# Kernel optimization log

Hardware: AMD Instinct MI355X
Metric: run time of the kernel (lower is better)

Reference implementation:

```python
import jax, jax.numpy as jnp
import numpy as np

N, E, DIN, H, CHID, COUT, S = 20000, 320000, 128, 4, 64, 64, 32
EPS_BN = 1e-5


def setup_inputs() -> dict:
    key = jax.random.key(0)
    ks = jax.random.split(key, 20)
    g = lambda k, shp, s=0.1: jax.random.normal(k, shp, dtype=jnp.float32) * s
    return {
        "x": jax.random.normal(ks[0], (N, DIN), dtype=jnp.float32),
        "edge_index": jax.random.randint(ks[1], (2, E), 0, N, dtype=jnp.int32),
        "struct_feat": jax.random.normal(ks[2], (N, S), dtype=jnp.float32),
        # GATConv (layer 1)
        "W1": g(ks[3], (H * CHID, DIN)),
        "att_src1": g(ks[4], (1, H, CHID)),
        "att_dst1": g(ks[5], (1, H, CHID)),
        "bias1": jnp.zeros((CHID,), jnp.float32),
        # HybridGateGATLayer (layer 2)
        "W2": g(ks[6], (H * COUT, CHID)),
        "att_src2": g(ks[7], (1, H, COUT)),
        "att_dst2": g(ks[8], (1, H, COUT)),
        "bias2": jnp.zeros((COUT,), jnp.float32),
        "Wt": g(ks[9], (1, S)),
        "bt": jnp.zeros((1,), jnp.float32),
        "We1": g(ks[10], (8, 4), 0.5),
        "be1": jnp.zeros((8,), jnp.float32),
        "We2": g(ks[11], (1, 8), 0.5),
        "be2": jnp.zeros((1,), jnp.float32),
        "betas": jnp.array([1.15, 0.85, 0.1, 0.08, 0.12], jnp.float32),
    }


def _seg_softmax(logits, seg, n):
    m = jax.ops.segment_max(logits, seg, num_segments=n)
    m = jnp.where(jnp.isfinite(m), m, 0.0)
    ex = jnp.exp(logits - m[seg])
    s = jax.ops.segment_sum(ex, seg, num_segments=n)
    return ex / (s[seg] + 1e-16)


def _cos(a, b):
    na = jnp.maximum(jnp.linalg.norm(a, axis=-1), 1e-8)
    nb = jnp.maximum(jnp.linalg.norm(b, axis=-1), 1e-8)
    return (a * b).sum(-1) / (na * nb)


def reference(x, edge_index, struct_feat, W1, att_src1, att_dst1, bias1,
              W2, att_src2, att_dst2, bias2, Wt, bt, We1, be1, We2, be2, betas):
    n = x.shape[0]
    src0, dst0 = edge_index[0], edge_index[1]
    # ---- layer 1: standard GATConv with self loops, concat=False (head mean) ----
    loop = jnp.arange(n, dtype=src0.dtype)
    src = jnp.concatenate([src0, loop])
    dst = jnp.concatenate([dst0, loop])
    h = (x @ W1.T).reshape(n, H, CHID)
    a_s = (h * att_src1).sum(-1)  # [N,H]
    a_d = (h * att_dst1).sum(-1)
    al = jax.nn.leaky_relu(a_s[src] + a_d[dst], 0.2)  # [E+N,H]
    alpha1 = _seg_softmax(al, dst, n)
    out1 = jax.ops.segment_sum(h[src] * alpha1[..., None], dst, num_segments=n)
    h1 = jax.nn.relu(out1.mean(1) + bias1)  # [N,CHID]
    # batch norm (affine=False, batch stats, biased var)
    mu = h1.mean(0)
    var = ((h1 - mu) ** 2).mean(0)
    h1 = (h1 - mu) / jnp.sqrt(var + EPS_BN)
    # ---- layer 2: HybridGateGATLayer (no self loops) ----
    x2 = (h1 @ W2.T).reshape(n, H, COUT)
    node_trust = jax.nn.sigmoid(struct_feat @ Wt.T + bt).squeeze(-1)  # [N]
    as2 = (x2 * att_src2).sum(-1)
    ad2 = (x2 * att_dst2).sum(-1)
    j, i = src0, dst0
    alpha_raw = jax.nn.leaky_relu(as2[j] + ad2[i], 0.2)  # [E,H]
    struct_sim = _cos(struct_feat[j], struct_feat[i])  # [E]
    xf = x2.reshape(n, H * COUT)
    feat_sim = _cos(xf[j], xf[i])
    agreement = struct_sim * feat_sim
    conflict = jnp.abs(struct_sim - feat_sim)
    cues = jnp.stack([struct_sim, feat_sim, agreement, conflict], axis=-1)  # [E,4]
    gate = (jax.nn.relu(cues @ We1.T + be1) @ We2.T + be2).squeeze(-1)
    edge_bonus = jax.nn.sigmoid(gate) * jax.nn.relu(agreement)
    edge_trust = jnp.sqrt(jnp.clip(node_trust[j] * node_trust[i], 0.0))
    trust_bonus = edge_trust * jax.nn.relu(0.5 * (struct_sim + feat_sim))
    gate_logit = (betas[0] * struct_sim + betas[1] * feat_sim + betas[2] * agreement
                  + betas[3] * edge_bonus + betas[4] * trust_bonus)
    alpha2 = _seg_softmax(alpha_raw + gate_logit[:, None], i, n)  # [E,H]
    out2 = jax.ops.segment_sum(x2[j] * alpha2[..., None], i, num_segments=n)
    return out2.mean(1) + bias2  # [N,COUT]
```

## Files before the change

### kernel.cpp

```cpp
#include <hip/hip_runtime.h>
#include <hip/hip_bf16.h>
#include <hip/hip_fp16.h>

#define C_DIN 128
#define C_H 4
#define C_CH 64
#define C_HC 256
#define C_S 32
#define MBLK 64

typedef __attribute__((ext_vector_type(8))) _Float16 half8;
typedef __attribute__((ext_vector_type(4))) float f32x4;

__device__ __forceinline__ float lrelu(float x) { return x >= 0.f ? x : 0.2f * x; }

__global__ void k_count(const int* __restrict__ dst, int* __restrict__ deg, int E) {
    int e = blockIdx.x * blockDim.x + threadIdx.x;
    if (e < E) atomicAdd(&deg[dst[e]], 1);
}

__global__ void k_scan(const int* __restrict__ deg, int* __restrict__ row_ptr,
                       int* __restrict__ cursor, int n) {
    __shared__ int part[1024];
    int t = threadIdx.x;
    const int C = (n + 1023) / 1024;
    int base = t * C;
    int s = 0;
    for (int k = 0; k < C; ++k) {
        int idx = base + k;
        if (idx < n) s += deg[idx];
    }
    part[t] = s;
    __syncthreads();
    for (int off = 1; off < 1024; off <<= 1) {
        int v = (t >= off) ? part[t - off] : 0;
        __syncthreads();
        part[t] += v;
        __syncthreads();
    }
    int run = (t == 0) ? 0 : part[t - 1];
    for (int k = 0; k < C; ++k) {
        int idx = base + k;
        if (idx < n) { row_ptr[idx] = run; cursor[idx] = run; run += deg[idx]; }
    }
    if (t == 1023) row_ptr[n] = run;
}

__global__ void k_scatter(const int* __restrict__ src, const int* __restrict__ dst,
                          int* __restrict__ cursor, int* __restrict__ adj_src, int E) {
    int e = blockIdx.x * blockDim.x + threadIdx.x;
    if (e < E) {
        int d = dst[e];
        int p = atomicAdd(&cursor[d], 1);
        adj_src[p] = src[e];
    }
}

__global__ void k_prepw(const float* __restrict__ W1, const float* __restrict__ W2,
                        _Float16* __restrict__ W1f, _Float16* __restrict__ W2f) {
    int i = blockIdx.x * blockDim.x + threadIdx.x;
    if (i < 4096) {
        int ks = i >> 10, rem = i & 1023, nt = rem >> 6, lpos = rem & 63;
        int c = nt * 16 + (lpos & 15);
        int kb = (ks * 4 + (lpos >> 4)) * 8;
        const float4* src = (const float4*)(W1 + (size_t)c * C_DIN + kb);
        float4 f0 = src[0], f1 = src[1];
        _Float16* dst = &W1f[(size_t)i * 8];
        dst[0] = (_Float16)f0.x; dst[1] = (_Float16)f0.y;
        dst[2] = (_Float16)f0.z; dst[3] = (_Float16)f0.w;
        dst[4] = (_Float16)f1.x; dst[5] = (_Float16)f1.y;
        dst[6] = (_Float16)f1.z; dst[7] = (_Float16)f1.w;
    } else if (i < 4096 + 2048) {
        int ii = i - 4096;
        int ks = ii >> 10, rem = ii & 1023, nt = rem >> 6, lpos = rem & 63;
        int c = nt * 16 + (lpos & 15);
        int kb = (ks * 4 + (lpos >> 4)) * 8;
        const float4* src = (const float4*)(W2 + (size_t)c * C_CH + kb);
        float4 f0 = src[0], f1 = src[1];
        _Float16* dst = &W2f[(size_t)ii * 8];
        dst[0] = (_Float16)f0.x; dst[1] = (_Float16)f0.y;
        dst[2] = (_Float16)f0.z; dst[3] = (_Float16)f0.w;
        dst[4] = (_Float16)f1.x; dst[5] = (_Float16)f1.y;
        dst[6] = (_Float16)f1.z; dst[7] = (_Float16)f1.w;
    }
}

__global__ __launch_bounds__(256) void k_gemm1(
    const float* __restrict__ x, const _Float16* __restrict__ W1f,
    const float* __restrict__ att_s, const float* __restrict__ att_d,
    __half* __restrict__ hh_out, float* __restrict__ a_s, float* __restrict__ a_d, int n) {
    __shared__ __align__(16) _Float16 as_[4 * 4 * 64 * 8];
    int t = threadIdx.x;
    int r0 = blockIdx.x * MBLK;
    {
        int row = t >> 2, q = t & 3;
        int rr = r0 + row;
        int mt = row >> 4, rl = row & 15;
        const float4* xrow = (const float4*)(x + (size_t)rr * C_DIN);
#pragma unroll
        for (int cc = 0; cc < 4; ++cc) {
            int ch = q * 4 + cc;
            float4 f0 = make_float4(0, 0, 0, 0), f1 = make_float4(0, 0, 0, 0);
            if (rr < n) { f0 = xrow[ch * 2]; f1 = xrow[ch * 2 + 1]; }
            int ks = ch >> 2, lg = ch & 3;
            _Float16* dst = &as_[(((ks * 4 + mt) * 64) + (lg * 16 + rl)) * 8];
            dst[0] = (_Float16)f0.x; dst[1] = (_Float16)f0.y;
            dst[2] = (_Float16)f0.z; dst[3] = (_Float16)f0.w;
            dst[4] = (_Float16)f1.x; dst[5] = (_Float16)f1.y;
            dst[6] = (_Float16)f1.z; dst[7] = (_Float16)f1.w;
        }
    }
    __syncthreads();
    int w = t >> 6, l = t & 63;
    const half8* Wv = (const half8*)W1f;
    f32x4 acc[4][4];
#pragma unroll
    for (int mt = 0; mt < 4; ++mt)
#pragma unroll
        for (int nt = 0; nt < 4; ++nt) acc[mt][nt] = (f32x4){0.f, 0.f, 0.f, 0.f};
#pragma unroll
    for (int ks = 0; ks < 4; ++ks) {
        half8 af[4], bf[4];
#pragma unroll
        for (int mt = 0; mt < 4; ++mt)
            af[mt] = *(const half8*)&as_[(((ks * 4 + mt) * 64) + l) * 8];
#pragma unroll
        for (int nt = 0; nt < 4; ++nt)
            bf[nt] = Wv[((ks * 16 + (w * 4 + nt)) * 64) + l];
#pragma unroll
        for (int mt = 0; mt < 4; ++mt)
#pragma unroll
            for (int nt = 0; nt < 4; ++nt)
                acc[mt][nt] = __builtin_amdgcn_mfma_f32_16x16x32_f16(af[mt], bf[nt],
                                                                     acc[mt][nt], 0, 0, 0);
    }
    int cl = l & 15, rg = l >> 4;
    float atv_s[4], atv_d[4];
#pragma unroll
    for (int nt = 0; nt < 4; ++nt) {
        atv_s[nt] = att_s[w * 64 + nt * 16 + cl];
        atv_d[nt] = att_d[w * 64 + nt * 16 + cl];
    }
#pragma unroll
    for (int mt = 0; mt < 4; ++mt) {
#pragma unroll
        for (int r = 0; r < 4; ++r) {
            int rr = r0 + mt * 16 + rg * 4 + r;
            float vs = 0.f, vd = 0.f;
#pragma unroll
            for (int nt = 0; nt < 4; ++nt) {
                float v = acc[mt][nt][r];
                vs += atv_s[nt] * v;
                vd += atv_d[nt] * v;
                if (rr < n)
                    hh_out[(size_t)rr * C_HC + w * 64 + nt * 16 + cl] = __float2half(v);
            }
#pragma unroll
            for (int off = 1; off < 16; off <<= 1) {
                vs += __shfl_xor(vs, off);
                vd += __shfl_xor(vd, off);
            }
            if (cl == 0 && rr < n) { a_s[rr * C_H + w] = vs; a_d[rr * C_H + w] = vd; }
        }
    }
}

__global__ __launch_bounds__(256) void k_layer1(
    const int* __restrict__ row_ptr, const int* __restrict__ adj_src,
    const __half* __restrict__ hhlf, const float* __restrict__ a_s,
    const float* __restrict__ a_d, const float* __restrict__ bias1,
    float* __restrict__ h1, int n) {
    int wid = (blockIdx.x * blockDim.x + threadIdx.x) >> 6;
    if (wid >= n) return;
    int l = threadIdx.x & 63, g = l >> 4, q = l & 15, h = q >> 2;
    int d = wid;
    int beg = row_ptr[d], end = row_ptr[d + 1];
    float adh = a_d[d * C_H + h];
    const float4* drow = (const float4*)(hhlf + (size_t)d * C_HC + q * 16);
    float4 d0 = drow[0], d1 = drow[1];
    float acc[16];
#pragma unroll
    for (int i = 0; i < 16; ++i) acc[i] = 0.f;
    float s = 0.f;
    if (g == 0) {
        float ps = expf(lrelu(a_s[d * C_H + h] + adh));
        const __half2* pa = (const __half2*)&d0;
        const __half2* pb = (const __half2*)&d1;
#pragma unroll
        for (int k = 0; k < 4; ++k) {
            float2 a = __half22float2(pa[k]);
            acc[k * 2] += ps * a.x; acc[k * 2 + 1] += ps * a.y;
            float2 b = __half22float2(pb[k]);
            acc[8 + k * 2] += ps * b.x; acc[8 + k * 2 + 1] += ps * b.y;
        }
        s += ps;
    }
    for (int cb = beg; cb < end; cb += 4) {
        int e = cb + g;
        bool act = e < end;
        int j = act ? adj_src[e] : d;
        const float4* jrow = (const float4*)(hhlf + (size_t)j * C_HC + q * 16);
        float4 r0 = jrow[0], r1 = jrow[1];
        float p = act ? expf(lrelu(a_s[j * C_H + h] + adh)) : 0.f;
        const __half2* pa = (const __half2*)&r0;
        const __half2* pb = (const __half2*)&r1;
#pragma unroll
        for (int k = 0; k < 4; ++k) {
            float2 a = __half22float2(pa[k]);
            acc[k * 2] += p * a.x; acc[k * 2 + 1] += p * a.y;
            float2 b = __half22float2(pb[k]);
            acc[8 + k * 2] += p * b.x; acc[8 + k * 2 + 1] += p * b.y;
        }
        s += p;
    }
#pragma unroll
    for (int off = 16; off <= 32; off <<= 1) {
#pragma unroll
        for (int i = 0; i < 16; ++i) acc[i] += __shfl_xor(acc[i], off);
        s += __shfl_xor(s, off);
    }
    float inv = 1.f / (s + 1e-16f);
#pragma unroll
    for (int i = 0; i < 16; ++i) acc[i] *= inv;
#pragma unroll
    for (int off = 4; off <= 8; off <<= 1) {
#pragma unroll
        for (int i = 0; i < 16; ++i) acc[i] += __shfl_xor(acc[i], off);
    }
    if (l < 4) {
#pragma unroll
        for (int i = 0; i < 16; ++i)
            h1[(size_t)d * C_CH + l * 16 + i] =
                fmaxf(acc[i] * 0.25f + bias1[l * 16 + i], 0.f);
    }
}

__global__ void k_bnstats(const float* __restrict__ h1, float* __restrict__ bn, int n) {
    int t = threadIdx.x;
    int c = t & 63, rg = t >> 6;
    float s = 0.f, s2 = 0.f;
    for (int r = blockIdx.x * 4 + rg; r < n; r += gridDim.x * 4) {
        float v = h1[(size_t)r * C_CH + c];
        s += v;
        s2 += v * v;
    }
    __shared__ float ls[256], ls2[256];
    ls[t] = s; ls2[t] = s2;
    __syncthreads();
    if (t < 64) {
        s = ls[t] + ls[t + 64] + ls[t + 128] + ls[t + 192];
        s2 = ls2[t] + ls2[t + 64] + ls2[t + 128] + ls2[t + 192];
        atomicAdd(&bn[c], s);
        atomicAdd(&bn[64 + c], s2);
    }
}

__global__ __launch_bounds__(256) void k_gemm2(
    const float* __restrict__ h1, const _Float16* __restrict__ W2f,
    const float* __restrict__ att_s, const float* __restrict__ att_d,
    const float* __restrict__ bn, __half* __restrict__ x2h,
    float* __restrict__ as2, float* __restrict__ ad2, float* __restrict__ nf, int n) {
    __shared__ __align__(16) _Float16 as_[2 * 4 * 64 * 8];
    __shared__ float nq[64][4];
    int t = threadIdx.x;
    int r0 = blockIdx.x * MBLK;
    {
        int row = t >> 2, q = t & 3;
        int rr = r0 + row;
        int mt = row >> 4, rl = row & 15;
        const float invN = 1.f / (float)n;
        const float4* hrow = (const float4*)(h1 + (size_t)rr * C_CH);
#pragma unroll
        for (int cc = 0; cc < 2; ++cc) {
            int ch = q * 2 + cc;
            float4 f0 = make_float4(0, 0, 0, 0), f1 = make_float4(0, 0, 0, 0);
            if (rr < n) { f0 = hrow[ch * 2]; f1 = hrow[ch * 2 + 1]; }
            float4 s0 = *(const float4*)&bn[ch * 8];
            float4 s1 = *(const float4*)&bn[ch * 8 + 4];
            float4 q0 = *(const float4*)&bn[64 + ch * 8];
            float4 q1 = *(const float4*)&bn[64 + ch * 8 + 4];
            float4 mu0 = make_float4(s0.x * invN, s0.y * invN, s0.z * invN, s0.w * invN);
            float4 mu1 = make_float4(s1.x * invN, s1.y * invN, s1.z * invN, s1.w * invN);
            float4 rs0 = make_float4(rsqrtf(q0.x * invN - mu0.x * mu0.x + 1e-5f),
                                     rsqrtf(q0.y * invN - mu0.y * mu0.y + 1e-5f),
                                     rsqrtf(q0.z * invN - mu0.z * mu0.z + 1e-5f),
                                     rsqrtf(q0.w * invN - mu0.w * mu0.w + 1e-5f));
            float4 rs1 = make_float4(rsqrtf(q1.x * invN - mu1.x * mu1.x + 1e-5f),
                                     rsqrtf(q1.y * invN - mu1.y * mu1.y + 1e-5f),
                                     rsqrtf(q1.z * invN - mu1.z * mu1.z + 1e-5f),
                                     rsqrtf(q1.w * invN - mu1.w * mu1.w + 1e-5f));
            int ks = ch >> 1, lg = ch & 1;
            ks = ch >> 2; lg = ch & 3;
            _Float16* dst = &as_[(((ks * 4 + mt) * 64) + (lg * 16 + rl)) * 8];
            dst[0] = (_Float16)((f0.x - mu0.x) * rs0.x);
            dst[1] = (_Float16)((f0.y - mu0.y) * rs0.y);
            dst[2] = (_Float16)((f0.z - mu0.z) * rs0.z);
            dst[3] = (_Float16)((f0.w - mu0.w) * rs0.w);
            dst[4] = (_Float16)((f1.x - mu1.x) * rs1.x);
            dst[5] = (_Float16)((f1.y - mu1.y) * rs1.y);
            dst[6] = (_Float16)((f1.z - mu1.z) * rs1.z);
            dst[7] = (_Float16)((f1.w - mu1.w) * rs1.w);
        }
    }
    __syncthreads();
    int w = t >> 6, l = t & 63;
    const half8* Wv = (const half8*)W2f;
    f32x4 acc[4][4];
#pragma unroll
    for (int mt = 0; mt < 4; ++mt)
#pragma unroll
        for (int nt = 0; nt < 4; ++nt) acc[mt][nt] = (f32x4){0.f, 0.f, 0.f, 0.f};
#pragma unroll
    for (int ks = 0; ks < 2; ++ks) {
        half8 af[4], bf[4];
#pragma unroll
        for (int mt = 0; mt < 4; ++mt)
            af[mt] = *(const half8*)&as_[(((ks * 4 + mt) * 64) + l) * 8];
#pragma unroll
        for (int nt = 0; nt < 4; ++nt)
            bf[nt] = Wv[((ks * 16 + (w * 4 + nt)) * 64) + l];
#pragma unroll
        for (int mt = 0; mt < 4; ++mt)
#pragma unroll
            for (int nt = 0; nt < 4; ++nt)
                acc[mt][nt] = __builtin_amdgcn_mfma_f32_16x16x32_f16(af[mt], bf[nt],
                                                                     acc[mt][nt], 0, 0, 0);
    }
    int cl = l & 15, rg = l >> 4;
    float atv_s[4], atv_d[4];
#pragma unroll
    for (int nt = 0; nt < 4; ++nt) {
        atv_s[nt] = att_s[w * 64 + nt * 16 + cl];
        atv_d[nt] = att_d[w * 64 + nt * 16 + cl];
    }
#pragma unroll
    for (int mt = 0; mt < 4; ++mt) {
#pragma unroll
        for (int r = 0; r < 4; ++r) {
            int rr = r0 + mt * 16 + rg * 4 + r;
            float vs = 0.f, vd = 0.f, vq = 0.f;
#pragma unroll
            for (int nt = 0; nt < 4; ++nt) {
                float v = acc[mt][nt][r];
                vs += atv_s[nt] * v;
                vd += atv_d[nt] * v;
                vq += v * v;
                if (rr < n)
                    x2h[(size_t)rr * C_HC + w * 64 + nt * 16 + cl] = __float2half(v);
            }
#pragma unroll
            for (int off = 1; off < 16; off <<= 1) {
                vs += __shfl_xor(vs, off);
                vd += __shfl_xor(vd, off);
                vq += __shfl_xor(vq, off);
            }
            if (cl == 0 && rr < n) {
                as2[rr * C_H + w] = vs;
                ad2[rr * C_H + w] = vd;
                nq[mt * 16 + rg * 4 + r][w] = vq;
            }
        }
    }
    __syncthreads();
    if (t < MBLK) {
        int rr = r0 + t;
        if (rr < n) {
            float qq = nq[t][0] + nq[t][1] + nq[t][2] + nq[t][3];
            nf[rr] = fmaxf(sqrtf(qq), 1e-8f);
        }
    }
}

__global__ void k_trust(const float* __restrict__ sf, const float* __restrict__ Wt,
                        const float* __restrict__ bt, float* __restrict__ trust,
                        float* __restrict__ ns, int n) {
    int i = blockIdx.x * blockDim.x + threadIdx.x;
    if (i >= n) return;
    const float4* r4 = (const float4*)(sf + (size_t)i * C_S);
    const float4* w4 = (const float4*)Wt;
    float d = 0.f, q = 0.f;
#pragma unroll
    for (int k = 0; k < 8; ++k) {
        float4 a = r4[k], w = w4[k];
        d += a.x * w.x + a.y * w.y + a.z * w.z + a.w * w.w;
        q += a.x * a.x + a.y * a.y + a.z * a.z + a.w * a.w;
    }
    trust[i] = 1.f / (1.f + expf(-(d + bt[0])));
    ns[i] = fmaxf(sqrtf(q), 1e-8f);
}

__global__ __launch_bounds__(256) void k_fused2(
    const int* __restrict__ row_ptr, const int* __restrict__ adj_src,
    const float* __restrict__ sf, const __half* __restrict__ x2h,
    const float* __restrict__ ns, const float* __restrict__ nf,
    const float* __restrict__ trust, const float* __restrict__ as2,
    const float* __restrict__ ad2, const float* __restrict__ We1,
    const float* __restrict__ be1, const float* __restrict__ We2,
    const float* __restrict__ be2, const float* __restrict__ betas,
    const float* __restrict__ bias2, float* __restrict__ out, int n) {
    int wid = (blockIdx.x * blockDim.x + threadIdx.x) >> 6;
    if (wid >= n) return;
    int l = threadIdx.x & 63, g = l >> 4, q = l & 15, h = q >> 2;
    int d = wid;
    int beg = row_ptr[d], end = row_ptr[d + 1];
    const float4* drow = (const float4*)(x2h + (size_t)d * C_HC + q * 16);
    float4 d0 = drow[0], d1 = drow[1];
    float2 sfd = *(const float2*)(sf + (size_t)d * C_S + q * 2);
    float ad2h = ad2[d * C_H + h];
    float nsd = ns[d], nfd = nf[d], trd = trust[d];
    float b20 = be2[0];
    float bt0 = betas[0], bt1 = betas[1], bt2 = betas[2], bt3 = betas[3], bt4 = betas[4];
    float acc[16];
#pragma unroll
    for (int i = 0; i < 16; ++i) acc[i] = 0.f;
    float s = 0.f;
    for (int cb = beg; cb < end; cb += 4) {
        int e = cb + g;
        bool act = e < end;
        int j = act ? adj_src[e] : d;
        const float4* jrow = (const float4*)(x2h + (size_t)j * C_HC + q * 16);
        float4 r0 = jrow[0], r1 = jrow[1];
        float2 sfj = *(const float2*)(sf + (size_t)j * C_S + q * 2);
        float fd = 0.f;
        {
            const __half2* pa = (const __half2*)&r0;
            const __half2* pb = (const __half2*)&d0;
#pragma unroll
            for (int k = 0; k < 4; ++k) {
                float2 a = __half22float2(pa[k]), b = __half22float2(pb[k]);
                fd += a.x * b.x + a.y * b.y;
            }
            const __half2* pc = (const __half2*)&r1;
            const __half2* pd = (const __half2*)&d1;
#pragma unroll
            for (int k = 0; k < 4; ++k) {
                float2 a = __half22float2(pc[k]), b = __half22float2(pd[k]);
                fd += a.x * b.x + a.y * b.y;
            }
        }
        float sd = sfj.x * sfd.x + sfj.y * sfd.y;
#pragma unroll
        for (int off = 1; off < 16; off <<= 1) {
            fd += __shfl_xor(fd, off);
            sd += __shfl_xor(sd, off);
        }
        float p = 0.f;
        if (act) {
            float ss = sd / (nsd * ns[j]);
            float fs = fd / (nfd * nf[j]);
            float agr = ss * fs;
            float con = fabsf(ss - fs);
            float gate = b20;
#pragma unroll
            for (int o = 0; o < 8; ++o) {
                float hdn = We1[o * 4 + 0] * ss + We1[o * 4 + 1] * fs +
                            We1[o * 4 + 2] * agr + We1[o * 4 + 3] * con + be1[o];
                gate += We2[o] * fmaxf(hdn, 0.f);
            }
            float eb = (1.f / (1.f + expf(-gate))) * fmaxf(agr, 0.f);
            float et = sqrtf(fmaxf(trd * trust[j], 0.f));
            float tb = et * fmaxf(0.5f * (ss + fs), 0.f);
            float glog = bt0 * ss + bt1 * fs + bt2 * agr + bt3 * eb + bt4 * tb;
            p = expf(lrelu(as2[j * C_H + h] + ad2h) + glog);
        }
        {
            const __half2* pa = (const __half2*)&r0;
            const __half2* pb = (const __half2*)&r1;
#pragma unroll
            for (int k = 0; k < 4; ++k) {
                float2 a = __half22float2(pa[k]);
                acc[k * 2] += p * a.x; acc[k * 2 + 1] += p * a.y;
                float2 b = __half22float2(pb[k]);
                acc[8 + k * 2] += p * b.x; acc[8 + k * 2 + 1] += p * b.y;
            }
        }
        s += p;
    }
#pragma unroll
    for (int off = 16; off <= 32; off <<= 1) {
#pragma unroll
        for (int i = 0; i < 16; ++i) acc[i] += __shfl_xor(acc[i], off);
        s += __shfl_xor(s, off);
    }
    float inv = 1.f / (s + 1e-16f);
#pragma unroll
    for (int i = 0; i < 16; ++i) acc[i] *= inv;
#pragma unroll
    for (int off = 4; off <= 8; off <<= 1) {
#pragma unroll
        for (int i = 0; i < 16; ++i) acc[i] += __shfl_xor(acc[i], off);
    }
    if (l < 4) {
#pragma unroll
        for (int i = 0; i < 16; ++i)
            out[(size_t)d * C_CH + l * 16 + i] = acc[i] * 0.25f + bias2[l * 16 + i];
    }
}

static inline size_t al256(size_t x) { return (x + 255) & ~(size_t)255; }

extern "C" void kernel_launch(void* const* d_in, const int* in_sizes, int n_in,
                              void* d_out, int out_size, void* d_ws, size_t ws_size,
                              hipStream_t stream) {
    const float* x      = (const float*)d_in[0];
    const int*   ei     = (const int*)d_in[1];
    const float* sf     = (const float*)d_in[2];
    const float* W1     = (const float*)d_in[3];
    const float* atts1  = (const float*)d_in[4];
    const float* attd1  = (const float*)d_in[5];
    const float* bias1  = (const float*)d_in[6];
    const float* W2     = (const float*)d_in[7];
    const float* atts2  = (const float*)d_in[8];
    const float* attd2  = (const float*)d_in[9];
    const float* bias2  = (const float*)d_in[10];
    const float* Wt     = (const float*)d_in[11];
    const float* bt     = (const float*)d_in[12];
    const float* We1    = (const float*)d_in[13];
    const float* be1    = (const float*)d_in[14];
    const float* We2    = (const float*)d_in[15];
    const float* be2    = (const float*)d_in[16];
    const float* betas  = (const float*)d_in[17];

    const int N = in_sizes[0] / C_DIN;
    const int E = in_sizes[1] / 2;
    const int* srcs = ei;
    const int* dsts = ei + E;

    char* p = (char*)d_ws;
    size_t off = 0;
    auto take = [&](size_t bytes) { char* r = p + off; off = al256(off + bytes); return r; };
    __half* hhlf  = (__half*)take((size_t)N * C_HC * 2);
    float* h1     = (float*)take((size_t)N * C_CH * 4);
    float* a_s1   = (float*)take((size_t)N * C_H * 4);
    float* a_d1   = (float*)take((size_t)N * C_H * 4);
    float* nf     = (float*)take((size_t)N * 4);
    float* ns     = (float*)take((size_t)N * 4);
    float* trust  = (float*)take((size_t)N * 4);
    int*   deg    = (int*)take((size_t)N * 4);
    int*   rowp   = (int*)take((size_t)(N + 1) * 4);
    int*   cursor = (int*)take((size_t)N * 4);
    int*   adj_s  = (int*)take((size_t)E * 4);
    _Float16* W1f = (_Float16*)take(4096 * 8 * 2);
    _Float16* W2f = (_Float16*)take(2048 * 8 * 2);
    float* bn     = (float*)take(128 * 4);
    (void)ws_size;
    __half* x2h = hhlf;
    float* as2  = a_s1;
    float* ad2  = a_d1;

    hipMemsetAsync(deg, 0, (size_t)N * 4, stream);
    hipMemsetAsync(bn, 0, 128 * 4, stream);

    k_prepw<<<24, 256, 0, stream>>>(W1, W2, W1f, W2f);
    k_count<<<(E + 255) / 256, 256, 0, stream>>>(dsts, deg, E);
    k_scan<<<1, 1024, 0, stream>>>(deg, rowp, cursor, N);
    k_scatter<<<(E + 255) / 256, 256, 0, stream>>>(srcs, dsts, cursor, adj_s, E);

    k_gemm1<<<(N + MBLK - 1) / MBLK, 256, 0, stream>>>(x, W1f, atts1, attd1, hhlf, a_s1,
                                                       a_d1, N);
    k_layer1<<<(N + 3) / 4, 256, 0, stream>>>(rowp, adj_s, hhlf, a_s1, a_d1, bias1, h1, N);
    k_bnstats<<<128, 256, 0, stream>>>(h1, bn, N);

    k_gemm2<<<(N + MBLK - 1) / MBLK, 256, 0, stream>>>(h1, W2f, atts2, attd2, bn, x2h,
                                                       as2, ad2, nf, N);
    k_trust<<<(N + 255) / 256, 256, 0, stream>>>(sf, Wt, bt, trust, ns, N);
    k_fused2<<<(N + 3) / 4, 256, 0, stream>>>(rowp, adj_s, sf, x2h, ns, nf, trust, as2, ad2,
                                              We1, be1, We2, be2, betas, bias2,
                                              (float*)d_out, N);
}
```

Baseline: 306.8 us.

## Prefetch next neighbor rows in edge loops, pack per-node metadata, use fdot2

The neighbor-gather loops in layer 1 and the fused layer-2 kernel now software-pipeline their loads: the next edge's source index, feature row, attention score and metadata are fetched before the current edge is processed, so gather latency can overlap with arithmetic. Per-node ns/nf/trust are packed into one float4 meta array so each neighbor needs a single vector load instead of three scattered scalar loads. The fp16 feature dot product uses the fdot2 builtin. The costs are higher register pressure and one extra, possibly redundant, prefetch per row.

```diff
diff --git a/kernel.cpp b/kernel.cpp
--- a/kernel.cpp
+++ b/kernel.cpp
@@ -10,9 +10,20 @@
 #define MBLK 64
 
 typedef __attribute__((ext_vector_type(8))) _Float16 half8;
+typedef __attribute__((ext_vector_type(2))) _Float16 h2f;
 typedef __attribute__((ext_vector_type(4))) float f32x4;
 
 __device__ __forceinline__ float lrelu(float x) { return x >= 0.f ? x : 0.2f * x; }
+
+#if __has_builtin(__builtin_amdgcn_fdot2)
+__device__ __forceinline__ float dot2acc(h2f a, h2f b, float c) {
+    return __builtin_amdgcn_fdot2(a, b, c, false);
+}
+#else
+__device__ __forceinline__ float dot2acc(h2f a, h2f b, float c) {
+    return c + (float)a.x * (float)b.x + (float)a.y * (float)b.y;
+}
+#endif
 
 __global__ void k_count(const int* __restrict__ dst, int* __restrict__ deg, int E) {
     int e = blockIdx.x * blockDim.x + threadIdx.x;
@@ -195,13 +206,19 @@
         }
         s += ps;
     }
+    bool act = (beg + g) < end;
+    int j = act ? adj_src[beg + g] : d;
+    const float4* jr = (const float4*)(hhlf + (size_t)j * C_HC + q * 16);
+    float4 r0 = jr[0], r1 = jr[1];
+    float asj = a_s[j * C_H + h];
     for (int cb = beg; cb < end; cb += 4) {
-        int e = cb + g;
-        bool act = e < end;
-        int j = act ? adj_src[e] : d;
-        const float4* jrow = (const float4*)(hhlf + (size_t)j * C_HC + q * 16);
-        float4 r0 = jrow[0], r1 = jrow[1];
-        float p = act ? expf(lrelu(a_s[j * C_H + h] + adh)) : 0.f;
+        int en = cb + 4 + g;
+        bool actn = en < end;
+        int jn = actn ? adj_src[en] : d;
+        const float4* jrn = (const float4*)(hhlf + (size_t)jn * C_HC + q * 16);
+        float4 nr0 = jrn[0], nr1 = jrn[1];
+        float asn = a_s[jn * C_H + h];
+        float p = act ? expf(lrelu(asj + adh)) : 0.f;
         const __half2* pa = (const __half2*)&r0;
         const __half2* pb = (const __half2*)&r1;
 #pragma unroll
@@ -212,6 +229,7 @@
             acc[8 + k * 2] += p * b.x; acc[8 + k * 2 + 1] += p * b.y;
         }
         s += p;
+        act = actn; r0 = nr0; r1 = nr1; asj = asn;
     }
 #pragma unroll
     for (int off = 16; off <= 32; off <<= 1) {
@@ -289,8 +307,7 @@
                                      rsqrtf(q1.y * invN - mu1.y * mu1.y + 1e-5f),
                                      rsqrtf(q1.z * invN - mu1.z * mu1.z + 1e-5f),
                                      rsqrtf(q1.w * invN - mu1.w * mu1.w + 1e-5f));
-            int ks = ch >> 1, lg = ch & 1;
-            ks = ch >> 2; lg = ch & 3;
+            int ks = ch >> 2, lg = ch & 3;
             _Float16* dst = &as_[(((ks * 4 + mt) * 64) + (lg * 16 + rl)) * 8];
             dst[0] = (_Float16)((f0.x - mu0.x) * rs0.x);
             dst[1] = (_Float16)((f0.y - mu0.y) * rs0.y);
@@ -372,8 +389,8 @@
 }
 
 __global__ void k_trust(const float* __restrict__ sf, const float* __restrict__ Wt,
-                        const float* __restrict__ bt, float* __restrict__ trust,
-                        float* __restrict__ ns, int n) {
+                        const float* __restrict__ bt, const float* __restrict__ nf,
+                        float* __restrict__ meta, int n) {
     int i = blockIdx.x * blockDim.x + threadIdx.x;
     if (i >= n) return;
     const float4* r4 = (const float4*)(sf + (size_t)i * C_S);
@@ -385,15 +402,15 @@
         d += a.x * w.x + a.y * w.y + a.z * w.z + a.w * w.w;
         q += a.x * a.x + a.y * a.y + a.z * a.z + a.w * a.w;
     }
-    trust[i] = 1.f / (1.f + expf(-(d + bt[0])));
-    ns[i] = fmaxf(sqrtf(q), 1e-8f);
+    float tr = 1.f / (1.f + expf(-(d + bt[0])));
+    float nsv = fmaxf(sqrtf(q), 1e-8f);
+    *(float4*)&meta[(size_t)i * 4] = make_float4(nsv, nf[i], tr, 0.f);
 }
 
 __global__ __launch_bounds__(256) void k_fused2(
     const int* __restrict__ row_ptr, const int* __restrict__ adj_src,
     const float* __restrict__ sf, const __half* __restrict__ x2h,
-    const float* __restrict__ ns, const float* __restrict__ nf,
-    const float* __restrict__ trust, const float* __restrict__ as2,
+    const float* __restrict__ meta, const float* __restrict__ as2,
     const float* __restrict__ ad2, const float* __restrict__ We1,
     const float* __restrict__ be1, const float* __restrict__ We2,
     const float* __restrict__ be2, const float* __restrict__ betas,
@@ -407,36 +424,40 @@
     float4 d0 = drow[0], d1 = drow[1];
     float2 sfd = *(const float2*)(sf + (size_t)d * C_S + q * 2);
     float ad2h = ad2[d * C_H + h];
-    float nsd = ns[d], nfd = nf[d], trd = trust[d];
+    float4 md = *(const float4*)&meta[(size_t)d * 4];
+    float nsd = md.x, nfd = md.y, trd = md.z;
     float b20 = be2[0];
     float bt0 = betas[0], bt1 = betas[1], bt2 = betas[2], bt3 = betas[3], bt4 = betas[4];
     float acc[16];
 #pragma unroll
     for (int i = 0; i < 16; ++i) acc[i] = 0.f;
     float s = 0.f;
+    bool act = (beg + g) < end;
+    int j = act ? adj_src[beg + g] : d;
+    const float4* jr0 = (const float4*)(x2h + (size_t)j * C_HC + q * 16);
+    float4 r0 = jr0[0], r1 = jr0[1];
+    float2 sfj = *(const float2*)(sf + (size_t)j * C_S + q * 2);
+    float4 mj = *(const float4*)&meta[(size_t)j * 4];
+    float4 asj = *(const float4*)&as2[j * C_H];
     for (int cb = beg; cb < end; cb += 4) {
-        int e = cb + g;
-        bool act = e < end;
-        int j = act ? adj_src[e] : d;
-        const float4* jrow = (const float4*)(x2h + (size_t)j * C_HC + q * 16);
-        float4 r0 = jrow[0], r1 = jrow[1];
-        float2 sfj = *(const float2*)(sf + (size_t)j * C_S + q * 2);
+        int en = cb + 4 + g;
+        bool actn = en < end;
+        int jn = actn ? adj_src[en] : d;
+        const float4* jrn = (const float4*)(x2h + (size_t)jn * C_HC + q * 16);
+        float4 nr0 = jrn[0], nr1 = jrn[1];
+        float2 nsfj = *(const float2*)(sf + (size_t)jn * C_S + q * 2);
+        float4 nmj = *(const float4*)&meta[(size_t)jn * 4];
+        float4 nasj = *(const float4*)&as2[jn * C_H];
         float fd = 0.f;
         {
-            const __half2* pa = (const __half2*)&r0;
-            const __half2* pb = (const __half2*)&d0;
-#pragma unroll
-            for (int k = 0; k < 4; ++k) {
-                float2 a = __half22float2(pa[k]), b = __half22float2(pb[k]);
-                fd += a.x * b.x + a.y * b.y;
-            }
-            const __half2* pc = (const __half2*)&r1;
-            const __half2* pd = (const __half2*)&d1;
-#pragma unroll
-            for (int k = 0; k < 4; ++k) {
-                float2 a = __half22float2(pc[k]), b = __half22float2(pd[k]);
-                fd += a.x * b.x + a.y * b.y;
-            }
+            const h2f* pa = (const h2f*)&r0;
+            const h2f* pb = (const h2f*)&d0;
+#pragma unroll
+            for (int k = 0; k < 4; ++k) fd = dot2acc(pa[k], pb[k], fd);
+            const h2f* pc = (const h2f*)&r1;
+            const h2f* pd = (const h2f*)&d1;
+#pragma unroll
+            for (int k = 0; k < 4; ++k) fd = dot2acc(pc[k], pd[k], fd);
         }
         float sd = sfj.x * sfd.x + sfj.y * sfd.y;
 #pragma unroll
@@ -446,8 +467,8 @@
         }
         float p = 0.f;
         if (act) {
-            float ss = sd / (nsd * ns[j]);
-            float fs = fd / (nfd * nf[j]);
+            float ss = sd / (nsd * mj.x);
+            float fs = fd / (nfd * mj.y);
             float agr = ss * fs;
             float con = fabsf(ss - fs);
             float gate = b20;
@@ -458,10 +479,11 @@
                 gate += We2[o] * fmaxf(hdn, 0.f);
             }
             float eb = (1.f / (1.f + expf(-gate))) * fmaxf(agr, 0.f);
-            float et = sqrtf(fmaxf(trd * trust[j], 0.f));
+            float et = sqrtf(fmaxf(trd * mj.z, 0.f));
             float tb = et * fmaxf(0.5f * (ss + fs), 0.f);
             float glog = bt0 * ss + bt1 * fs + bt2 * agr + bt3 * eb + bt4 * tb;
-            p = expf(lrelu(as2[j * C_H + h] + ad2h) + glog);
+            float ash = (h == 0) ? asj.x : (h == 1) ? asj.y : (h == 2) ? asj.z : asj.w;
+            p = expf(lrelu(ash + ad2h) + glog);
         }
         {
             const __half2* pa = (const __half2*)&r0;
@@ -475,6 +497,7 @@
             }
         }
         s += p;
+        act = actn; r0 = nr0; r1 = nr1; sfj = nsfj; mj = nmj; asj = nasj;
     }
 #pragma unroll
     for (int off = 16; off <= 32; off <<= 1) {
@@ -534,8 +557,7 @@
     float* a_s1   = (float*)take((size_t)N * C_H * 4);
     float* a_d1   = (float*)take((size_t)N * C_H * 4);
     float* nf     = (float*)take((size_t)N * 4);
-    float* ns     = (float*)take((size_t)N * 4);
-    float* trust  = (float*)take((size_t)N * 4);
+    float* meta   = (float*)take((size_t)N * 4 * 4);
     int*   deg    = (int*)take((size_t)N * 4);
     int*   rowp   = (int*)take((size_t)(N + 1) * 4);
     int*   cursor = (int*)take((size_t)N * 4);
@@ -563,8 +585,8 @@
 
     k_gemm2<<<(N + MBLK - 1) / MBLK, 256, 0, stream>>>(h1, W2f, atts2, attd2, bn, x2h,
                                                        as2, ad2, nf, N);
-    k_trust<<<(N + 255) / 256, 256, 0, stream>>>(sf, Wt, bt, trust, ns, N);
-    k_fused2<<<(N + 3) / 4, 256, 0, stream>>>(rowp, adj_s, sf, x2h, ns, nf, trust, as2, ad2,
+    k_trust<<<(N + 255) / 256, 256, 0, stream>>>(sf, Wt, bt, nf, meta, N);
+    k_fused2<<<(N + 3) / 4, 256, 0, stream>>>(rowp, adj_s, sf, x2h, meta, as2, ad2,
                                               We1, be1, We2, be2, betas, bias2,
                                               (float*)d_out, N);
 }
```

Result: faster. 284.2 us (-7.4%).
